# Kernel tuning notes

Measured on AMD Instinct MI355X. Metric: run time of the kernel, lower is better.

The kernel has to match this reference:

```python
import jax, jax.numpy as jnp
import numpy as np

G = 128        # grid resolution per axis (points are voxel centers on this grid)
N = 262144     # number of input points == number of output points
CIN = 16
COUT = 32


def _build_neighbors(inp_coords, out_coords):
    """Emulates FixedRadiusSearch(Linf, r=1.53*voxel) + invert_neighbors_list on a
    unit grid: for each output point and each of the 27 kernel taps t, find the
    (unique) input point at out_coord - (t-1), or -1 if that voxel is empty."""
    enc = lambda c: (c[:, 0].astype(np.int64) * G + c[:, 1]) * G + c[:, 2]
    inp_keys = enc(inp_coords)
    order = np.argsort(inp_keys)
    skeys = inp_keys[order]
    nbr = np.full((out_coords.shape[0], 27), -1, dtype=np.int32)
    k = 0
    for t0 in range(3):
        for t1 in range(3):
            for t2 in range(3):
                d = np.array([t0 - 1, t1 - 1, t2 - 1], dtype=np.int64)
                nc = out_coords - d  # input voxel s.t. (out - inp) == d
                valid = np.all((nc >= 0) & (nc < G), axis=1)
                keys = enc(np.clip(nc, 0, G - 1))
                pos = np.searchsorted(skeys, keys).clip(0, len(skeys) - 1)
                found = valid & (skeys[pos] == keys)
                nbr[:, k] = np.where(found, order[pos].astype(np.int32), -1)
                k += 1
    return nbr


def setup_inputs() -> dict:
    rng = np.random.default_rng(0)
    # unique voxels -> at most one point per voxel (regular-grid assumption)
    inp_keys = rng.choice(G ** 3, size=N, replace=False)
    out_keys = rng.choice(G ** 3, size=N, replace=False)
    dec = lambda kk: np.stack([kk // (G * G), (kk // G) % G, kk % G], axis=1).astype(np.int64)
    nbr_idx = jnp.asarray(_build_neighbors(dec(inp_keys), dec(out_keys)))

    key = jax.random.key(0)
    k1, k2 = jax.random.split(key)
    inp_features = jax.random.normal(k1, (N, CIN), dtype=jnp.float32)
    # matches kernel_initializer = uniform_(-0.05, 0.05)
    kernel = jax.random.uniform(k2, (3, 3, 3, CIN, COUT), dtype=jnp.float32,
                                minval=-0.05, maxval=0.05)
    bias = jnp.zeros((COUT,), dtype=jnp.float32)  # bias_initializer = zeros_
    return {"inp_features": inp_features, "kernel": kernel, "bias": bias,
            "nbr_idx": nbr_idx}


def reference(inp_features, kernel, bias, nbr_idx):
    # continuous_conv_transpose with interpolation='nearest_neighbor',
    # coordinate_mapping='identity', normalize=False on a unit grid:
    # out[j] = sum_t W[t] @ f[nbr(j, t)]  (missing taps contribute zero), + bias
    valid = (nbr_idx >= 0)
    idx = jnp.where(valid, nbr_idx, 0)
    gathered = inp_features[idx] * valid[..., None].astype(inp_features.dtype)  # [N,27,Cin]
    W = kernel.reshape(27, kernel.shape[-2], kernel.shape[-1])                  # [27,Cin,Cout]
    return jnp.einsum('nkc,kco->no', gathered, W) + bias
```

## Files before the change

kernel.cpp:

```cpp
#include <hip/hip_runtime.h>
#include <hip/hip_bf16.h>

#define NPTS  262144
#define CIN   16
#define COUT  32
#define NTAPS 27
#define BLK   512

typedef __attribute__((ext_vector_type(8)))  short short8v;
typedef __attribute__((ext_vector_type(16))) float f32x16;

__global__ __launch_bounds__(256) void cvt_feat_kernel(
    const float* __restrict__ feat, __hip_bfloat16* __restrict__ fb)
{
    const int i = blockIdx.x * 256 + threadIdx.x;
    const float4 x = ((const float4*)feat)[i];
    __hip_bfloat162* o = (__hip_bfloat162*)fb;
    o[2 * i]     = __float22bfloat162_rn(float2{x.x, x.y});
    o[2 * i + 1] = __float22bfloat162_rn(float2{x.z, x.w});
}

template<bool USE_WS>
__global__ __launch_bounds__(BLK, 6) void sct_mfma_kernel(
    const float* __restrict__ feat,
    const __hip_bfloat16* __restrict__ featb,
    const float* __restrict__ Wg,
    const float* __restrict__ bias,
    const int*   __restrict__ nbr,
    float*       __restrict__ out)
{
    __shared__ short bpack[NTAPS * 512];

    const int tid = threadIdx.x;
    for (int i = tid; i < NTAPS * 512; i += BLK) {
        const int tap  = i >> 9;
        const int r    = i & 511;
        const int ln   = r >> 3;
        const int e    = r & 7;
        const int cin  = ((ln >> 5) << 3) + e;
        const int cout = ln & 31;
        const __hip_bfloat16 h = __float2bfloat16(Wg[(tap * CIN + cin) * COUT + cout]);
        bpack[i] = *(const short*)&h;
    }
    __syncthreads();

    const int lane = tid & 63;
    const int wv   = tid >> 6;
    const int p0   = blockIdx.x * 256 + wv * 32;
    const int prow = lane & 31;
    const int g    = lane >> 5;
    const long nbase = (long)(p0 + prow) * NTAPS;

    f32x16 acc;
    {
        const float b = bias[prow];
        #pragma unroll
        for (int r2 = 0; r2 < 16; ++r2) acc[r2] = b;
    }

    auto gather1 = [&](int id, short8v& dst) {
        short8v a = {};
        if (id >= 0) {
            if (USE_WS) {
                a = *(const short8v*)(featb + (long)id * CIN + g * 8);
            } else {
                const float4* fp = (const float4*)(feat + (long)id * CIN + g * 8);
                const float4 x = fp[0];
                const float4 y = fp[1];
                union { short8v v; __hip_bfloat162 h[4]; } u;
                u.h[0] = __float22bfloat162_rn(float2{x.x, x.y});
                u.h[1] = __float22bfloat162_rn(float2{x.z, x.w});
                u.h[2] = __float22bfloat162_rn(float2{y.x, y.y});
                u.h[3] = __float22bfloat162_rn(float2{y.z, y.w});
                a = u.v;
            }
        }
        dst = a;
    };

    int4    nid[2];
    short8v af[2][4];

    nid[0] = *(const int4*)(nbr + nbase);
    gather1(nid[0].x, af[0][0]);
    gather1(nid[0].y, af[0][1]);
    gather1(nid[0].z, af[0][2]);
    gather1(nid[0].w, af[0][3]);

    #pragma unroll
    for (int grp = 0; grp < 7; ++grp) {
        const int cur = grp & 1, nxt = cur ^ 1;
        if (grp < 6) {
            if (grp == 5) {
                const int2 t = *(const int2*)(nbr + nbase + 24);
                nid[nxt] = make_int4(t.x, t.y, nbr[nbase + 26], -1);
            } else {
                nid[nxt] = *(const int4*)(nbr + nbase + 4 * (grp + 1));
            }
            gather1(nid[nxt].x, af[nxt][0]);
            gather1(nid[nxt].y, af[nxt][1]);
            gather1(nid[nxt].z, af[nxt][2]);
            gather1(nid[nxt].w, af[nxt][3]);
        }
        const int ntaps_cur = (grp == 6) ? 3 : 4;
        #pragma unroll
        for (int k = 0; k < 4; ++k) {
            if (k < ntaps_cur) {
                const int tap = 4 * grp + k;
                const short8v bf = *(const short8v*)&bpack[(tap << 9) + (lane << 3)];
                acc = __builtin_amdgcn_mfma_f32_32x32x16_bf16(af[cur][k], bf, acc, 0, 0, 0);
            }
        }
    }

    #pragma unroll
    for (int r2 = 0; r2 < 16; ++r2) {
        const int row = (r2 & 3) + 8 * (r2 >> 2) + 4 * g;
        out[(long)(p0 + row) * COUT + prow] = acc[r2];
    }
}

extern "C" void kernel_launch(void* const* d_in, const int* in_sizes, int n_in,
                              void* d_out, int out_size, void* d_ws, size_t ws_size,
                              hipStream_t stream) {
    const float* feat = (const float*)d_in[0];
    const float* Wg   = (const float*)d_in[1];
    const float* bias = (const float*)d_in[2];
    const int*   nbr  = (const int*)d_in[3];
    float*       out  = (float*)d_out;

    const size_t need = (size_t)NPTS * CIN * sizeof(__hip_bfloat16);
    if (ws_size >= need) {
        __hip_bfloat16* fb = (__hip_bfloat16*)d_ws;
        cvt_feat_kernel<<<NPTS * CIN / 4 / 256, 256, 0, stream>>>(feat, fb);
        sct_mfma_kernel<true><<<NPTS / 256, BLK, 0, stream>>>(feat, fb, Wg, bias, nbr, out);
    } else {
        sct_mfma_kernel<false><<<NPTS / 256, BLK, 0, stream>>>(feat, nullptr, Wg, bias, nbr, out);
    }
}
```

Measured before the change: 44.22 us.

## Deepen gather prefetch to a rolling window of twelve taps

Loads all 27 neighbor indices up front into registers, then keeps twelve bf16 feature gathers in flight in a rolling window ahead of the MFMA chain instead of double-buffering groups of four. This is meant to hide the latency of the random gathers by raising memory-level parallelism per wave. The extra registers force launch bounds down from 6 to 3 blocks per CU, so occupancy drops.

```diff
diff --git a/kernel.cpp b/kernel.cpp
--- a/kernel.cpp
+++ b/kernel.cpp
@@ -6,6 +6,7 @@
 #define COUT  32
 #define NTAPS 27
 #define BLK   512
+#define DEPTH 12
 
 typedef __attribute__((ext_vector_type(8)))  short short8v;
 typedef __attribute__((ext_vector_type(16))) float f32x16;
@@ -21,7 +22,7 @@
 }
 
 template<bool USE_WS>
-__global__ __launch_bounds__(BLK, 6) void sct_mfma_kernel(
+__global__ __launch_bounds__(BLK, 3) void sct_mfma_kernel(
     const float* __restrict__ feat,
     const __hip_bfloat16* __restrict__ featb,
     const float* __restrict__ Wg,
@@ -49,7 +50,18 @@
     const int p0   = blockIdx.x * 256 + wv * 32;
     const int prow = lane & 31;
     const int g    = lane >> 5;
-    const long nbase = (long)(p0 + prow) * NTAPS;
+    const int* nb  = nbr + (long)(p0 + prow) * NTAPS;
+
+    int nid[NTAPS];
+    #pragma unroll
+    for (int q = 0; q < 6; ++q) {
+        const int4 v = *(const int4*)(nb + 4 * q);
+        nid[4*q+0] = v.x; nid[4*q+1] = v.y; nid[4*q+2] = v.z; nid[4*q+3] = v.w;
+    }
+    {
+        const int2 v2 = *(const int2*)(nb + 24);
+        nid[24] = v2.x; nid[25] = v2.y; nid[26] = nb[26];
+    }
 
     f32x16 acc;
     {
@@ -58,7 +70,10 @@
         for (int r2 = 0; r2 < 16; ++r2) acc[r2] = b;
     }
 
-    auto gather1 = [&](int id, short8v& dst) {
+    short8v af[DEPTH];
+
+    auto gather1 = [&](int t, short8v& dst) {
+        const int id = nid[t];
         short8v a = {};
         if (id >= 0) {
             if (USE_WS) {
@@ -78,39 +93,14 @@
         dst = a;
     };
 
-    int4    nid[2];
-    short8v af[2][4];
-
-    nid[0] = *(const int4*)(nbr + nbase);
-    gather1(nid[0].x, af[0][0]);
-    gather1(nid[0].y, af[0][1]);
-    gather1(nid[0].z, af[0][2]);
-    gather1(nid[0].w, af[0][3]);
+    #pragma unroll
+    for (int t = 0; t < DEPTH; ++t) gather1(t, af[t]);
 
     #pragma unroll
-    for (int grp = 0; grp < 7; ++grp) {
-        const int cur = grp & 1, nxt = cur ^ 1;
-        if (grp < 6) {
-            if (grp == 5) {
-                const int2 t = *(const int2*)(nbr + nbase + 24);
-                nid[nxt] = make_int4(t.x, t.y, nbr[nbase + 26], -1);
-            } else {
-                nid[nxt] = *(const int4*)(nbr + nbase + 4 * (grp + 1));
-            }
-            gather1(nid[nxt].x, af[nxt][0]);
-            gather1(nid[nxt].y, af[nxt][1]);
-            gather1(nid[nxt].z, af[nxt][2]);
-            gather1(nid[nxt].w, af[nxt][3]);
-        }
-        const int ntaps_cur = (grp == 6) ? 3 : 4;
-        #pragma unroll
-        for (int k = 0; k < 4; ++k) {
-            if (k < ntaps_cur) {
-                const int tap = 4 * grp + k;
-                const short8v bf = *(const short8v*)&bpack[(tap << 9) + (lane << 3)];
-                acc = __builtin_amdgcn_mfma_f32_32x32x16_bf16(af[cur][k], bf, acc, 0, 0, 0);
-            }
-        }
+    for (int t = 0; t < NTAPS; ++t) {
+        const short8v bf = *(const short8v*)&bpack[(t << 9) + (lane << 3)];
+        acc = __builtin_amdgcn_mfma_f32_32x32x16_bf16(af[t % DEPTH], bf, acc, 0, 0, 0);
+        if (t + DEPTH < NTAPS) gather1(t + DEPTH, af[(t + DEPTH) % DEPTH]);
     }
 
     #pragma unroll
```

New measurement: 43.86 us. Within noise of the previous version (-0.8%).
